# Kernel tuning notes

Measured on AMD Instinct MI355X. Metric: run time of the kernel, lower is better.

The kernel has to match this reference:

```python
import jax, jax.numpy as jnp
import numpy as np

SOS_IDX, EOS_IDX, PAD_IDX = 0, 1, 59
NEG = -10000.0


def setup_inputs() -> dict:
    B, T, K = 256, 512, 128
    key = jax.random.key(0)
    k1, k2, k3 = jax.random.split(key, 3)
    h = jax.random.normal(k1, (B, T, K), dtype=jnp.float32)
    trans = jax.random.normal(k2, (K, K), dtype=jnp.float32)
    # replicate the constructor's masking of forbidden transitions
    trans = (trans.at[SOS_IDX, :].set(NEG)
                  .at[:, EOS_IDX].set(NEG)
                  .at[:, PAD_IDX].set(NEG)
                  .at[PAD_IDX, :].set(NEG)
                  .at[PAD_IDX, EOS_IDX].set(0.0)
                  .at[PAD_IDX, PAD_IDX].set(0.0))
    # monotone 0/1 float mask from random valid lengths (as a real CRF batch has)
    lengths = jax.random.randint(k3, (B,), 1, T + 1)
    mask = (jnp.arange(T)[None, :] < lengths[:, None]).astype(jnp.float32)
    return {"h": h, "trans": trans, "mask": mask}


def reference(h, trans, mask):
    # h: [B, T, K] emissions; trans: [K, K] (trans[i, j] = score j -> i); mask: [B, T]
    B, T, K = h.shape
    init = jnp.full((B, K), NEG, dtype=h.dtype).at[:, SOS_IDX].set(0.0)

    def step(score, xs):
        h_t, m_t = xs  # [B, K], [B]
        # score[:, None, :] + emit[:, :, None] + trans -> logsumexp over prev tag
        new = jax.nn.logsumexp(score[:, None, :] + h_t[:, :, None] + trans[None], axis=-1)
        m = m_t[:, None]
        return new * m + score * (1.0 - m), None

    score, _ = jax.lax.scan(step, init, (jnp.swapaxes(h, 0, 1), mask.T))
    return jax.nn.logsumexp(score + trans[EOS_IDX], axis=-1)  # [B]
```

## Files before the change

kernel.cpp:

```cpp
#include <hip/hip_runtime.h>

#define NEGV -10000.0f
constexpr int K  = 128;
constexpr int T  = 512;
constexpr int CH = 8;

typedef float f32x2 __attribute__((ext_vector_type(2)));
typedef float f32x4 __attribute__((ext_vector_type(4)));

__device__ __forceinline__ void bar_lgkm() {
  asm volatile("s_waitcnt lgkmcnt(0)\n\ts_barrier" ::: "memory");
}
template <int CTRL>
__device__ __forceinline__ float dpp_add(float x) {
  int o = __builtin_amdgcn_update_dpp(0, __float_as_int(x), CTRL, 0xF, 0xF, true);
  return x + __int_as_float(o);
}
__device__ __forceinline__ float sum8(float x) {
  x = dpp_add<0xB1>(x);
  x = dpp_add<0x4E>(x);
  x = dpp_add<0x141>(x);
  return x;
}

#if __has_builtin(__builtin_elementwise_fma)
#define VFMA(a, b, c) __builtin_elementwise_fma((a), (b), (c))
#else
__device__ __forceinline__ f32x2 VFMA(f32x2 a, f32x2 b, f32x2 c) {
  f32x2 r; r.x = fmaf(a.x, b.x, c.x); r.y = fmaf(a.y, b.y, c.y); return r;
}
#endif

__global__ __attribute__((amdgpu_flat_work_group_size(256, 256),
                          amdgpu_waves_per_eu(1, 1)))
void crf_fwd(const float* __restrict__ h, const float* __restrict__ trans,
             const float* __restrict__ mask, float* __restrict__ out) {
  const int tid  = threadIdx.x;
  const int b    = blockIdx.x;
  const int wid  = tid >> 6;
  const int lane = tid & 63;
  const int gl   = lane >> 3;
  const int oct  = lane & 7;
  const int sb   = 4 * (8 * wid + gl);
  const int rot  = oct >> 1;
  const int k0   = 16 * oct + 4 * ((0 + rot) & 3);
  const int k1   = 16 * oct + 4 * ((1 + rot) & 3);
  const int k2   = 16 * oct + 4 * ((2 + rot) & 3);
  const int k3   = 16 * oct + 4 * ((3 + rot) & 3);

  __shared__ __align__(16) float p_lds[2][K];
  __shared__ float Mslot[2];
  __shared__ float red[8];

  float msum = mask[b * T + tid] + mask[b * T + 256 + tid];
  #pragma unroll
  for (int off = 32; off > 0; off >>= 1) msum += __shfl_xor(msum, off);
  if (lane == 0) red[wid] = msum;

#define EXP4(v) v.x = __expf(v.x); v.y = __expf(v.y); \
                v.z = __expf(v.z); v.w = __expf(v.w);
#define LDE(si) \
  const float* rp##si = trans + (size_t)(sb + si) * K; \
  f32x4 w##si##0 = *reinterpret_cast<const f32x4*>(rp##si + k0); \
  f32x4 w##si##1 = *reinterpret_cast<const f32x4*>(rp##si + k1); \
  f32x4 w##si##2 = *reinterpret_cast<const f32x4*>(rp##si + k2); \
  f32x4 w##si##3 = *reinterpret_cast<const f32x4*>(rp##si + k3); \
  EXP4(w##si##0) EXP4(w##si##1) EXP4(w##si##2) EXP4(w##si##3) \
  f32x2 E##si##0l = __builtin_shufflevector(w##si##0, w##si##0, 0, 1); \
  f32x2 E##si##0h = __builtin_shufflevector(w##si##0, w##si##0, 2, 3); \
  f32x2 E##si##1l = __builtin_shufflevector(w##si##1, w##si##1, 0, 1); \
  f32x2 E##si##1h = __builtin_shufflevector(w##si##1, w##si##1, 2, 3); \
  f32x2 E##si##2l = __builtin_shufflevector(w##si##2, w##si##2, 0, 1); \
  f32x2 E##si##2h = __builtin_shufflevector(w##si##2, w##si##2, 2, 3); \
  f32x2 E##si##3l = __builtin_shufflevector(w##si##3, w##si##3, 0, 1); \
  f32x2 E##si##3h = __builtin_shufflevector(w##si##3, w##si##3, 2, 3);
  LDE(0) LDE(1) LDE(2) LDE(3)
#undef LDE
#undef EXP4
#define PIN(si) asm volatile("" : "+v"(E##si##0l), "+v"(E##si##0h), \
    "+v"(E##si##1l), "+v"(E##si##1h), "+v"(E##si##2l), "+v"(E##si##2h), \
    "+v"(E##si##3l), "+v"(E##si##3h));
  PIN(0) PIN(1) PIN(2) PIN(3)
#undef PIN
  const f32x4 trE = *reinterpret_cast<const f32x4*>(trans + K + sb);

  const float* hT = h + (size_t)b * T * K + sb;
  f32x4 hA0, hA1, hA2, hA3, hA4, hA5, hA6, hA7;
  f32x4 hB0 = {0,0,0,0}, hB1 = {0,0,0,0}, hB2 = {0,0,0,0}, hB3 = {0,0,0,0},
        hB4 = {0,0,0,0}, hB5 = {0,0,0,0}, hB6 = {0,0,0,0}, hB7 = {0,0,0,0};
#define LDH(BUF, t0) \
  BUF##0 = *reinterpret_cast<const f32x4*>(hT + (size_t)((t0) + 0) * K); \
  BUF##1 = *reinterpret_cast<const f32x4*>(hT + (size_t)((t0) + 1) * K); \
  BUF##2 = *reinterpret_cast<const f32x4*>(hT + (size_t)((t0) + 2) * K); \
  BUF##3 = *reinterpret_cast<const f32x4*>(hT + (size_t)((t0) + 3) * K); \
  BUF##4 = *reinterpret_cast<const f32x4*>(hT + (size_t)((t0) + 4) * K); \
  BUF##5 = *reinterpret_cast<const f32x4*>(hT + (size_t)((t0) + 5) * K); \
  BUF##6 = *reinterpret_cast<const f32x4*>(hT + (size_t)((t0) + 6) * K); \
  BUF##7 = *reinterpret_cast<const f32x4*>(hT + (size_t)((t0) + 7) * K); \
  asm volatile("" : "+v"(BUF##0), "+v"(BUF##1), "+v"(BUF##2), "+v"(BUF##3), \
                    "+v"(BUF##4), "+v"(BUF##5), "+v"(BUF##6), "+v"(BUF##7));
  LDH(hA, 0)

  if (tid < K) p_lds[0][tid] = (tid == 0) ? 1.0f : 0.0f;
  if (tid < 2) Mslot[tid] = 0.0f;
  bar_lgkm();

  const int len = (int)(red[0] + red[1] + red[2] + red[3] + 0.5f);
  const int nch = (len + CH - 1) >> 3;

  float Scur = 0.0f;
  float fsA = NEGV, fsB = NEGV, fsC = NEGV, fsD = NEGV;

#define STEP(cc, CUR, NXT, MC, BASE)                                         \
  if ((BASE) + (cc) < len) {                                                 \
    bar_lgkm();                          \
    float Snext = Scur;                                                      \
    if ((cc) == 0) {                                         \
      if (MC) Snext = Mslot[(MC) & 1];                                       \
      if ((BASE) + CH < len) { LDH(NXT, (BASE) + CH) }         \
    }                                                                        \
    const f32x4 hv4 = CUR##cc;                                               \
    const float* pb = p_lds[(cc) & 1];                                       \
    const f32x4 qq0 = *reinterpret_cast<const f32x4*>(pb + k0);              \
    const f32x4 qq1 = *reinterpret_cast<const f32x4*>(pb + k1);              \
    const f32x4 qq2 = *reinterpret_cast<const f32x4*>(pb + k2);              \
    const f32x4 qq3 = *reinterpret_cast<const f32x4*>(pb + k3);              \
    const f32x2 q0l = __builtin_shufflevector(qq0, qq0, 0, 1);               \
    const f32x2 q0h = __builtin_shufflevector(qq0, qq0, 2, 3);               \
    const f32x2 q1l = __builtin_shufflevector(qq1, qq1, 0, 1);               \
    const f32x2 q1h = __builtin_shufflevector(qq1, qq1, 2, 3);               \
    const f32x2 q2l = __builtin_shufflevector(qq2, qq2, 0, 1);               \
    const f32x2 q2h = __builtin_shufflevector(qq2, qq2, 2, 3);               \
    const f32x2 q3l = __builtin_shufflevector(qq3, qq3, 0, 1);               \
    const f32x2 q3h = __builtin_shufflevector(qq3, qq3, 2, 3);               \
    DOTSI(0) DOTSI(1) DOTSI(2) DOTSI(3)                                      \
    const float dsh = Scur - Snext;          \
    if (oct == 0) {                                                          \
      f32x4 pw;                                                              \
      pw.x = tot0 * __expf(hv4.x + dsh);                                     \
      pw.y = tot1 * __expf(hv4.y + dsh);                                     \
      pw.z = tot2 * __expf(hv4.z + dsh);                                     \
      pw.w = tot3 * __expf(hv4.w + dsh);                                     \
      *reinterpret_cast<f32x4*>(&p_lds[((cc) & 1) ^ 1][sb]) = pw;            \
    }                                                                        \
    if ((cc) == CH - 1 || (BASE) + (cc) == len - 1) {                        \
      fsA = hv4.x + Scur + __logf(tot0);                                     \
      fsB = hv4.y + Scur + __logf(tot1);                                     \
      fsC = hv4.z + Scur + __logf(tot2);                                     \
      fsD = hv4.w + Scur + __logf(tot3);                                     \
      if (tid == 0) Mslot[((MC) + 1) & 1] = fsC;      \
    }                                                                        \
    Scur = Snext;                                                            \
  }

#define DOTSI(si) \
      f32x2 u##si = {0.f, 0.f}, v##si = {0.f, 0.f}; \
      u##si = VFMA(E##si##0l, q0l, u##si); v##si = VFMA(E##si##0h, q0h, v##si); \
      u##si = VFMA(E##si##1l, q1l, u##si); v##si = VFMA(E##si##1h, q1h, v##si); \
      u##si = VFMA(E##si##2l, q2l, u##si); v##si = VFMA(E##si##2h, q2h, v##si); \
      u##si = VFMA(E##si##3l, q3l, u##si); v##si = VFMA(E##si##3h, q3h, v##si); \
      const float tot##si = sum8((u##si.x + u##si.y) + (v##si.x + v##si.y));

#define CHUNK(CUR, NXT, MC, BASE)                                            \
  { STEP(0, CUR, NXT, MC, BASE) STEP(1, CUR, NXT, MC, BASE)                  \
    STEP(2, CUR, NXT, MC, BASE) STEP(3, CUR, NXT, MC, BASE)                  \
    STEP(4, CUR, NXT, MC, BASE) STEP(5, CUR, NXT, MC, BASE)                  \
    STEP(6, CUR, NXT, MC, BASE) STEP(7, CUR, NXT, MC, BASE) }

  for (int mc = 0; mc < nch; mc += 2) {
    CHUNK(hA, hB, mc, mc << 3)
    if (mc + 1 < nch) { CHUNK(hB, hA, mc + 1, (mc + 1) << 3) }
  }
#undef CHUNK
#undef DOTSI
#undef STEP
#undef LDH

  f32x4 ff;
  ff.x = fsA + trE.x; ff.y = fsB + trE.y;
  ff.z = fsC + trE.z; ff.w = fsD + trE.w;
  float mx = fmaxf(fmaxf(ff.x, ff.y), fmaxf(ff.z, ff.w));
  #pragma unroll
  for (int off = 32; off > 0; off >>= 1) mx = fmaxf(mx, __shfl_xor(mx, off));
  if (lane == 0) red[wid] = mx;
  bar_lgkm();
  const float fm = fmaxf(fmaxf(red[0], red[1]), fmaxf(red[2], red[3]));
  float e = 0.0f;
  if (oct == 0)
    e = (__expf(ff.x - fm) + __expf(ff.y - fm)) +
        (__expf(ff.z - fm) + __expf(ff.w - fm));
  #pragma unroll
  for (int off = 32; off > 0; off >>= 1) e += __shfl_xor(e, off);
  if (lane == 0) red[4 + wid] = e;
  bar_lgkm();
  if (tid == 0) out[b] = fm + __logf((red[4] + red[5]) + (red[6] + red[7]));
}

extern "C" void kernel_launch(void* const* d_in, const int* in_sizes, int n_in,
                              void* d_out, int out_size, void* d_ws, size_t ws_size,
                              hipStream_t stream) {
  const float* h     = (const float*)d_in[0];
  const float* trans = (const float*)d_in[1];
  const float* mask  = (const float*)d_in[2];
  float* out = (float*)d_out;
  const int B = in_sizes[0] / (T * K);
  crf_fwd<<<B, 256, 0, stream>>>(h, trans, mask, out);
}
```

Before: 273.9 us.

## Spread per-tag epilogue across four lanes and precompute exp(h) off critical path

Each group of eight lanes now has four lanes own one output tag each, instead of one lane writing all four tags. Emission exponentials are computed ahead of time, interleaved into steps 3 and 5 of the previous chunk, and kept as one selected scalar per lane instead of a float4, which cuts register pressure. The rescale factor for the running maximum is applied as a multiply on step 0, and the chunk maximum now comes from tid 2's log value. This shortens the serial per-step tail but adds select logic and a changed rescaling order that could affect numerical behaviour.

New measurement: 256.1 us. 1.07x faster.

```diff
diff --git a/kernel.cpp b/kernel.cpp
--- a/kernel.cpp
+++ b/kernel.cpp
@@ -47,6 +47,8 @@
   const int k1   = 16 * oct + 4 * ((1 + rot) & 3);
   const int k2   = 16 * oct + 4 * ((2 + rot) & 3);
   const int k3   = 16 * oct + 4 * ((3 + rot) & 3);
+  const bool o1f = (oct & 1) != 0;
+  const bool o2f = (oct & 2) != 0;
 
   __shared__ __align__(16) float p_lds[2][K];
   __shared__ float Mslot[2];
@@ -76,30 +78,40 @@
   f32x2 E##si##3h = __builtin_shufflevector(w##si##3, w##si##3, 2, 3);
   LDE(0) LDE(1) LDE(2) LDE(3)
 #undef LDE
-#undef EXP4
 #define PIN(si) asm volatile("" : "+v"(E##si##0l), "+v"(E##si##0h), \
     "+v"(E##si##1l), "+v"(E##si##1h), "+v"(E##si##2l), "+v"(E##si##2h), \
     "+v"(E##si##3l), "+v"(E##si##3h));
   PIN(0) PIN(1) PIN(2) PIN(3)
 #undef PIN
-  const f32x4 trE = *reinterpret_cast<const f32x4*>(trans + K + sb);
 
   const float* hT = h + (size_t)b * T * K + sb;
-  f32x4 hA0, hA1, hA2, hA3, hA4, hA5, hA6, hA7;
-  f32x4 hB0 = {0,0,0,0}, hB1 = {0,0,0,0}, hB2 = {0,0,0,0}, hB3 = {0,0,0,0},
-        hB4 = {0,0,0,0}, hB5 = {0,0,0,0}, hB6 = {0,0,0,0}, hB7 = {0,0,0,0};
-#define LDH(BUF, t0) \
-  BUF##0 = *reinterpret_cast<const f32x4*>(hT + (size_t)((t0) + 0) * K); \
-  BUF##1 = *reinterpret_cast<const f32x4*>(hT + (size_t)((t0) + 1) * K); \
-  BUF##2 = *reinterpret_cast<const f32x4*>(hT + (size_t)((t0) + 2) * K); \
-  BUF##3 = *reinterpret_cast<const f32x4*>(hT + (size_t)((t0) + 3) * K); \
-  BUF##4 = *reinterpret_cast<const f32x4*>(hT + (size_t)((t0) + 4) * K); \
-  BUF##5 = *reinterpret_cast<const f32x4*>(hT + (size_t)((t0) + 5) * K); \
-  BUF##6 = *reinterpret_cast<const f32x4*>(hT + (size_t)((t0) + 6) * K); \
-  BUF##7 = *reinterpret_cast<const f32x4*>(hT + (size_t)((t0) + 7) * K); \
-  asm volatile("" : "+v"(BUF##0), "+v"(BUF##1), "+v"(BUF##2), "+v"(BUF##3), \
-                    "+v"(BUF##4), "+v"(BUF##5), "+v"(BUF##6), "+v"(BUF##7));
-  LDH(hA, 0)
+  f32x4 ld0, ld1, ld2, ld3, ld4, ld5, ld6, ld7;
+  float sA0, sA1, sA2, sA3, sA4, sA5, sA6, sA7;
+  float sB0, sB1, sB2, sB3, sB4, sB5, sB6, sB7;
+#define LDH(t0) \
+  ld0 = *reinterpret_cast<const f32x4*>(hT + (size_t)((t0) + 0) * K); \
+  ld1 = *reinterpret_cast<const f32x4*>(hT + (size_t)((t0) + 1) * K); \
+  ld2 = *reinterpret_cast<const f32x4*>(hT + (size_t)((t0) + 2) * K); \
+  ld3 = *reinterpret_cast<const f32x4*>(hT + (size_t)((t0) + 3) * K); \
+  ld4 = *reinterpret_cast<const f32x4*>(hT + (size_t)((t0) + 4) * K); \
+  ld5 = *reinterpret_cast<const f32x4*>(hT + (size_t)((t0) + 5) * K); \
+  ld6 = *reinterpret_cast<const f32x4*>(hT + (size_t)((t0) + 6) * K); \
+  ld7 = *reinterpret_cast<const f32x4*>(hT + (size_t)((t0) + 7) * K); \
+  asm volatile("" : "+v"(ld0), "+v"(ld1), "+v"(ld2), "+v"(ld3), \
+                    "+v"(ld4), "+v"(ld5), "+v"(ld6), "+v"(ld7));
+#define EXPSEL(c, DST) { \
+    f32x4 e_; \
+    e_.x = __expf(ld##c.x); e_.y = __expf(ld##c.y); \
+    e_.z = __expf(ld##c.z); e_.w = __expf(ld##c.w); \
+    const float lo_ = o1f ? e_.y : e_.x; \
+    const float hi_ = o1f ? e_.w : e_.z; \
+    DST = o2f ? hi_ : lo_; \
+    asm volatile("" : "+v"(DST)); }
+#define SELH03(P) EXPSEL(0, P##0) EXPSEL(1, P##1) EXPSEL(2, P##2) EXPSEL(3, P##3)
+#define SELH47(P) EXPSEL(4, P##4) EXPSEL(5, P##5) EXPSEL(6, P##6) EXPSEL(7, P##7)
+
+  LDH(0)
+  SELH03(sA) SELH47(sA)
 
   if (tid < K) p_lds[0][tid] = (tid == 0) ? 1.0f : 0.0f;
   if (tid < 2) Mslot[tid] = 0.0f;
@@ -109,17 +121,25 @@
   const int nch = (len + CH - 1) >> 3;
 
   float Scur = 0.0f;
-  float fsA = NEGV, fsB = NEGV, fsC = NEGV, fsD = NEGV;
-
-#define STEP(cc, CUR, NXT, MC, BASE)                                         \
+  float fsS  = NEGV;
+
+#define DOTSI(si) \
+      f32x2 u##si = {0.f, 0.f}, v##si = {0.f, 0.f}; \
+      u##si = VFMA(E##si##0l, q0l, u##si); v##si = VFMA(E##si##0h, q0h, v##si); \
+      u##si = VFMA(E##si##1l, q1l, u##si); v##si = VFMA(E##si##1h, q1h, v##si); \
+      u##si = VFMA(E##si##2l, q2l, u##si); v##si = VFMA(E##si##2h, q2h, v##si); \
+      u##si = VFMA(E##si##3l, q3l, u##si); v##si = VFMA(E##si##3h, q3h, v##si); \
+      const float tot##si = sum8((u##si.x + u##si.y) + (v##si.x + v##si.y));
+
+#define STEP(cc, CURS, NXTS, MC, BASE)                                       \
   if ((BASE) + (cc) < len) {                                                 \
     bar_lgkm();                          \
     float Snext = Scur;                                                      \
-    if ((cc) == 0) {                                         \
-      if (MC) Snext = Mslot[(MC) & 1];                                       \
-      if ((BASE) + CH < len) { LDH(NXT, (BASE) + CH) }         \
+    float dsf   = 1.0f;                                                      \
+    if ((cc) == 0 && (MC)) {                                                 \
+      Snext = Mslot[(MC) & 1];                                               \
+      dsf   = __expf(Scur - Snext);    \
     }                                                                        \
-    const f32x4 hv4 = CUR##cc;                                               \
     const float* pb = p_lds[(cc) & 1];                                       \
     const f32x4 qq0 = *reinterpret_cast<const f32x4*>(pb + k0);              \
     const f32x4 qq1 = *reinterpret_cast<const f32x4*>(pb + k1);              \
@@ -134,61 +154,50 @@
     const f32x2 q3l = __builtin_shufflevector(qq3, qq3, 0, 1);               \
     const f32x2 q3h = __builtin_shufflevector(qq3, qq3, 2, 3);               \
     DOTSI(0) DOTSI(1) DOTSI(2) DOTSI(3)                                      \
-    const float dsh = Scur - Snext;          \
-    if (oct == 0) {                                                          \
-      f32x4 pw;                                                              \
-      pw.x = tot0 * __expf(hv4.x + dsh);                                     \
-      pw.y = tot1 * __expf(hv4.y + dsh);                                     \
-      pw.z = tot2 * __expf(hv4.z + dsh);                                     \
-      pw.w = tot3 * __expf(hv4.w + dsh);                                     \
-      *reinterpret_cast<f32x4*>(&p_lds[((cc) & 1) ^ 1][sb]) = pw;            \
-    }                                                                        \
+                 \
+    const float tlo = o1f ? tot1 : tot0;                                     \
+    const float thi = o1f ? tot3 : tot2;                                     \
+    float pwo = (o2f ? thi : tlo) * CURS##cc;                                \
+    if ((cc) == 0) pwo *= dsf;                                               \
+    if (oct < 4) p_lds[((cc) & 1) ^ 1][sb + oct] = pwo;                      \
+    if ((cc) == 0 && (BASE) + CH < len) { LDH((BASE) + CH) }                 \
+    if ((cc) == 3 && (BASE) + CH < len) { SELH03(NXTS) }                     \
+    if ((cc) == 5 && (BASE) + CH < len) { SELH47(NXTS) }                     \
     if ((cc) == CH - 1 || (BASE) + (cc) == len - 1) {                        \
-      fsA = hv4.x + Scur + __logf(tot0);                                     \
-      fsB = hv4.y + Scur + __logf(tot1);                                     \
-      fsC = hv4.z + Scur + __logf(tot2);                                     \
-      fsD = hv4.w + Scur + __logf(tot3);                                     \
-      if (tid == 0) Mslot[((MC) + 1) & 1] = fsC;      \
+      fsS = __logf(pwo) + Snext;            \
+      if (tid == 2) Mslot[((MC) + 1) & 1] = fsS;      \
     }                                                                        \
     Scur = Snext;                                                            \
   }
 
-#define DOTSI(si) \
-      f32x2 u##si = {0.f, 0.f}, v##si = {0.f, 0.f}; \
-      u##si = VFMA(E##si##0l, q0l, u##si); v##si = VFMA(E##si##0h, q0h, v##si); \
-      u##si = VFMA(E##si##1l, q1l, u##si); v##si = VFMA(E##si##1h, q1h, v##si); \
-      u##si = VFMA(E##si##2l, q2l, u##si); v##si = VFMA(E##si##2h, q2h, v##si); \
-      u##si = VFMA(E##si##3l, q3l, u##si); v##si = VFMA(E##si##3h, q3h, v##si); \
-      const float tot##si = sum8((u##si.x + u##si.y) + (v##si.x + v##si.y));
-
-#define CHUNK(CUR, NXT, MC, BASE)                                            \
-  { STEP(0, CUR, NXT, MC, BASE) STEP(1, CUR, NXT, MC, BASE)                  \
-    STEP(2, CUR, NXT, MC, BASE) STEP(3, CUR, NXT, MC, BASE)                  \
-    STEP(4, CUR, NXT, MC, BASE) STEP(5, CUR, NXT, MC, BASE)                  \
-    STEP(6, CUR, NXT, MC, BASE) STEP(7, CUR, NXT, MC, BASE) }
+#define CHUNK(CURS, NXTS, MC, BASE)                                          \
+  { STEP(0, CURS, NXTS, MC, BASE) STEP(1, CURS, NXTS, MC, BASE)              \
+    STEP(2, CURS, NXTS, MC, BASE) STEP(3, CURS, NXTS, MC, BASE)              \
+    STEP(4, CURS, NXTS, MC, BASE) STEP(5, CURS, NXTS, MC, BASE)              \
+    STEP(6, CURS, NXTS, MC, BASE) STEP(7, CURS, NXTS, MC, BASE) }
 
   for (int mc = 0; mc < nch; mc += 2) {
-    CHUNK(hA, hB, mc, mc << 3)
-    if (mc + 1 < nch) { CHUNK(hB, hA, mc + 1, (mc + 1) << 3) }
+    CHUNK(sA, sB, mc, mc << 3)
+    if (mc + 1 < nch) { CHUNK(sB, sA, mc + 1, (mc + 1) << 3) }
   }
 #undef CHUNK
+#undef STEP
 #undef DOTSI
-#undef STEP
+#undef SELH03
+#undef SELH47
+#undef EXPSEL
 #undef LDH
-
-  f32x4 ff;
-  ff.x = fsA + trE.x; ff.y = fsB + trE.y;
-  ff.z = fsC + trE.z; ff.w = fsD + trE.w;
-  float mx = fmaxf(fmaxf(ff.x, ff.y), fmaxf(ff.z, ff.w));
+#undef EXP4
+
+  const float trEo = trans[K + sb + (oct & 3)];
+  const float ffv = (oct < 4) ? (fsS + trEo) : NEGV;
+  float mx = ffv;
   #pragma unroll
   for (int off = 32; off > 0; off >>= 1) mx = fmaxf(mx, __shfl_xor(mx, off));
   if (lane == 0) red[wid] = mx;
   bar_lgkm();
   const float fm = fmaxf(fmaxf(red[0], red[1]), fmaxf(red[2], red[3]));
-  float e = 0.0f;
-  if (oct == 0)
-    e = (__expf(ff.x - fm) + __expf(ff.y - fm)) +
-        (__expf(ff.z - fm) + __expf(ff.w - fm));
+  float e = (oct < 4) ? __expf(ffv - fm) : 0.0f;
   #pragma unroll
   for (int off = 32; off > 0; off >>= 1) e += __shfl_xor(e, off);
   if (lane == 0) red[4 + wid] = e;
```
